# Kernel optimization log

Hardware: AMD Instinct MI355X
Metric: run time of the kernel (lower is better)

Reference implementation:

```python
import jax, jax.numpy as jnp
import numpy as np

DIM = 512
NUM_HEADS = 8
WINDOW = 8
HEAD_DIM = DIM // NUM_HEADS
SCALE = HEAD_DIM ** -0.5


def setup_inputs() -> dict:
    key = jax.random.key(0)
    ks = jax.random.split(key, 6)
    B, S, C = 16, 4096, DIM
    hidden_states = jax.random.normal(ks[0], (B, S, C), dtype=jnp.float32)
    attn_output = jnp.zeros((1,), dtype=jnp.float32)  # unused positional arg in original __call__
    # nn.Linear params stored as (in, out) for y = x @ W + b
    qkv_w = jax.random.normal(ks[1], (C, 3 * C), dtype=jnp.float32) * (C ** -0.5)
    qkv_b = jnp.zeros((3 * C,), dtype=jnp.float32)
    proj_w = jax.random.normal(ks[2], (C, C), dtype=jnp.float32) * (C ** -0.5)
    proj_b = jnp.zeros((C,), dtype=jnp.float32)
    return {
        "attn_output": attn_output,
        "hidden_states": hidden_states,
        "qkv_w": qkv_w,
        "qkv_b": qkv_b,
        "proj_w": proj_w,
        "proj_b": proj_b,
    }


def reference(attn_output, hidden_states, qkv_w, qkv_b, proj_w, proj_b):
    B, S, C = hidden_states.shape
    h = w = int(np.sqrt(S))
    ws = WINDOW
    nh, hd = NUM_HEADS, HEAD_DIM
    # [B, S, C] -> [B, h, w, C]; h, w divisible by ws so no padding needed.
    x = hidden_states.reshape(B, h, w, C)
    # window partition -> [B, Nwin, T, C], T = ws*ws
    x = x.reshape(B, h // ws, ws, w // ws, ws, C)
    x = x.transpose(0, 1, 3, 2, 4, 5).reshape(B, (h // ws) * (w // ws), ws * ws, C)
    Nwin, T = x.shape[1], x.shape[2]
    # QKV projection
    qkv = x @ qkv_w + qkv_b                      # [B, Nwin, T, 3C]
    qkv = qkv.reshape(B, Nwin, T, 3, nh, hd)
    q, k, v = qkv[..., 0, :, :], qkv[..., 1, :, :], qkv[..., 2, :, :]  # [B, Nwin, T, nh, hd]
    # attention within each window
    attn = jnp.einsum('bwthd,bwshd->bwhts', q, k) * SCALE
    attn = jax.nn.softmax(attn, axis=-1)
    out = jnp.einsum('bwhts,bwshd->bwthd', attn, v).reshape(B, Nwin, T, C)
    out = out @ proj_w + proj_b
    # window reassembly -> [B, h, w, C]
    out = out.reshape(B, h // ws, w // ws, ws, ws, C)
    out = out.transpose(0, 1, 3, 2, 4, 5).reshape(B, h, w, C)
    return out.reshape(B, S, C)
```

## Files before the change

### kernel.cpp

```cpp
#include <hip/hip_runtime.h>
#include <stdint.h>

typedef __attribute__((ext_vector_type(8))) __bf16 v8bf;
typedef __attribute__((ext_vector_type(4))) __bf16 v4bf;
typedef __attribute__((ext_vector_type(4))) float  v4f;

#define SCALE 0.125f

__device__ __forceinline__ unsigned short f2bf(float f) {
  unsigned u = __float_as_uint(f);
  u += 0x7fffu + ((u >> 16) & 1u);
  return (unsigned short)(u >> 16);
}

__global__ void __launch_bounds__(256) k_transpose_cast(
    const float* __restrict__ in, unsigned short* __restrict__ out, int K, int N) {
  __shared__ float tile[64][65];
  const int t  = threadIdx.x;
  const int kt = blockIdx.x * 64;
  const int nt = blockIdx.y * 64;
  {
    int kl = t >> 2;
    int c0 = (t & 3) * 16;
    const float* src = in + (size_t)(kt + kl) * N + nt + c0;
#pragma unroll
    for (int i = 0; i < 16; i += 4) {
      float4 v = *(const float4*)(src + i);
      tile[kl][c0 + i + 0] = v.x; tile[kl][c0 + i + 1] = v.y;
      tile[kl][c0 + i + 2] = v.z; tile[kl][c0 + i + 3] = v.w;
    }
  }
  __syncthreads();
  {
    int nl = t >> 2;
    int k0 = (t & 3) * 16;
    unsigned short* dst = out + (size_t)(nt + nl) * K + kt + k0;
#pragma unroll
    for (int i = 0; i < 16; ++i) dst[i] = f2bf(tile[k0 + i][nl]);
  }
}

__global__ void __launch_bounds__(256) k_gather_cast(
    const float* __restrict__ x, unsigned short* __restrict__ xg) {
  const int t  = threadIdx.x;
  const int m  = blockIdx.x * 4 + (t >> 6);
  const int i0 = (t & 63) * 8;
  const int b = m >> 12, r = m & 4095, win = r >> 6, tt = r & 63;
  const int y  = ((win >> 3) << 3) + (tt >> 3);
  const int xx = ((win & 7) << 3) + (tt & 7);
  const size_t s = ((size_t)b << 12) + (size_t)y * 64 + xx;
  const float4* src = (const float4*)(x + s * 512 + i0);
  float4 a = src[0], c = src[1];
  unsigned u0 = (unsigned)f2bf(a.x) | ((unsigned)f2bf(a.y) << 16);
  unsigned u1 = (unsigned)f2bf(a.z) | ((unsigned)f2bf(a.w) << 16);
  unsigned u2 = (unsigned)f2bf(c.x) | ((unsigned)f2bf(c.y) << 16);
  unsigned u3 = (unsigned)f2bf(c.z) | ((unsigned)f2bf(c.w) << 16);
  *(int4*)(xg + (size_t)m * 512 + i0) = make_int4((int)u0, (int)u1, (int)u2, (int)u3);
}

__device__ __forceinline__ void stage_tile(const unsigned short* g, int row0, int k0,
                                           unsigned short* s, int tid) {
#pragma unroll
  for (int p = 0; p < 2; ++p) {
    int o = p * 4096 + tid * 16;
    const char* src = (const char*)g + (((size_t)(row0 + (o >> 6))) << 10) + (k0 << 1) + (o & 63);
    char* dst = (char*)s + p * 4096 + (tid & ~63) * 16;
    __builtin_amdgcn_global_load_lds((const __attribute__((address_space(1))) void*)src,
                                     (__attribute__((address_space(3))) void*)dst, 16, 0, 0);
  }
}

__device__ __forceinline__ void gemm_core(const unsigned short* A, const unsigned short* Bt,
                                          int rowBase, int colBase,
                                          unsigned short* sA, unsigned short* sB,
                                          v4f acc[4][4]) {
  const int tid = threadIdx.x;
  const int lane = tid & 63, wid = tid >> 6;
  const int wr = wid >> 1, wc = wid & 1;
  const int la = lane & 15, lb = lane >> 4;
#pragma unroll 1
  for (int kt = 0; kt < 16; ++kt) {
    const int k0 = kt * 32;
    stage_tile(A,  rowBase, k0, sA, tid);
    stage_tile(Bt, colBase, k0, sB, tid);
    asm volatile("s_waitcnt vmcnt(0)" ::: "memory");
    __syncthreads();
    v8bf af[4], bf_[4];
#pragma unroll
    for (int m = 0; m < 4; ++m)
      af[m] = *(const v8bf*)&sA[(wr * 64 + m * 16 + la) * 32 + lb * 8];
#pragma unroll
    for (int n = 0; n < 4; ++n)
      bf_[n] = *(const v8bf*)&sB[(wc * 64 + n * 16 + la) * 32 + lb * 8];
#pragma unroll
    for (int m = 0; m < 4; ++m)
#pragma unroll
      for (int n = 0; n < 4; ++n)
        acc[m][n] = __builtin_amdgcn_mfma_f32_16x16x32_bf16(af[m], bf_[n], acc[m][n], 0, 0, 0);
    __syncthreads();
  }
}

__global__ void __launch_bounds__(256) k_gemm_qkv(
    const unsigned short* __restrict__ A, const unsigned short* __restrict__ Bt,
    const float* __restrict__ bias, unsigned short* __restrict__ C) {
  __shared__ unsigned short sA[128 * 32];
  __shared__ unsigned short sB[128 * 32];
  const int bid = blockIdx.x;
  const int b2 = (bid & 7) * 768 + (bid >> 3);
  const int tm = b2 / 12, tn = b2 % 12;
  const int rowBase = tm * 128, colBase = tn * 128;
  v4f acc[4][4] = {};
  gemm_core(A, Bt, rowBase, colBase, sA, sB, acc);
  const int tid = threadIdx.x, lane = tid & 63, wid = tid >> 6;
  const int wr = wid >> 1, wc = wid & 1, la = lane & 15, lb = lane >> 4;
#pragma unroll
  for (int n = 0; n < 4; ++n) {
    const int col = colBase + wc * 64 + n * 16 + la;
    const float bv = bias[col];
#pragma unroll
    for (int m = 0; m < 4; ++m)
#pragma unroll
      for (int j = 0; j < 4; ++j) {
        const size_t row = (size_t)rowBase + wr * 64 + m * 16 + lb * 4 + j;
        C[row * 1536 + col] = f2bf(acc[m][n][j] + bv);
      }
  }
}

__global__ void __launch_bounds__(256) k_gemm_proj(
    const unsigned short* __restrict__ A, const unsigned short* __restrict__ Bt,
    const float* __restrict__ bias, float* __restrict__ out) {
  __shared__ unsigned short sA[128 * 32];
  __shared__ unsigned short sB[128 * 32];
  const int bid = blockIdx.x;
  const int b2 = (bid & 7) * 256 + (bid >> 3);
  const int tm = b2 >> 2, tn = b2 & 3;
  const int rowBase = tm * 128, colBase = tn * 128;
  v4f acc[4][4] = {};
  gemm_core(A, Bt, rowBase, colBase, sA, sB, acc);
  const int tid = threadIdx.x, lane = tid & 63, wid = tid >> 6;
  const int wr = wid >> 1, wc = wid & 1, la = lane & 15, lb = lane >> 4;
#pragma unroll
  for (int m = 0; m < 4; ++m) {
#pragma unroll
    for (int j = 0; j < 4; ++j) {
      const int row = rowBase + wr * 64 + m * 16 + lb * 4 + j;
      const int b = row >> 12, r = row & 4095, win = r >> 6, tt = r & 63;
      const int y  = ((win >> 3) << 3) + (tt >> 3);
      const int xx = ((win & 7) << 3) + (tt & 7);
      const size_t srow = ((size_t)b << 12) + (size_t)y * 64 + xx;
      float* orow = out + srow * 512;
#pragma unroll
      for (int n = 0; n < 4; ++n) {
        const int col = colBase + wc * 64 + n * 16 + la;
        orow[col] = acc[m][n][j] + bias[col];
      }
    }
  }
}

__global__ void __launch_bounds__(256) k_attn(
    const unsigned short* __restrict__ QKV, unsigned short* __restrict__ O) {
  __shared__ unsigned short sQ[64 * 72];
  __shared__ unsigned short sK[64 * 72];
  __shared__ unsigned short sP[64 * 72];
  __shared__ unsigned short sVt[64 * 68];
  const int bid = blockIdx.x;
  const int b = bid >> 9, win = (bid >> 3) & 63, head = bid & 7;
  const size_t m0 = ((size_t)b << 12) + (size_t)win * 64;
  const int tid = threadIdx.x, lane = tid & 63, w = tid >> 6;
  const int la = lane & 15, lb = lane >> 4;

  {
    const int rowl = tid >> 2;
    const unsigned short* qrow = QKV + (m0 + rowl) * 1536;
#pragma unroll
    for (int p = 0; p < 2; ++p) {
      const int seg = (tid & 3) + p * 4;
      int4 vq = *(const int4*)(qrow + head * 64 + seg * 8);
      *(int4*)&sQ[rowl * 72 + seg * 8] = vq;
      int4 vk = *(const int4*)(qrow + 512 + head * 64 + seg * 8);
      *(int4*)&sK[rowl * 72 + seg * 8] = vk;
      int4 vv = *(const int4*)(qrow + 1024 + head * 64 + seg * 8);
      const unsigned short* pv = (const unsigned short*)&vv;
#pragma unroll
      for (int i = 0; i < 8; ++i)
        sVt[(seg * 8 + i) * 68 + rowl] = pv[i];
    }
  }
  __syncthreads();

  v4f sc[4] = {};
#pragma unroll
  for (int kk = 0; kk < 2; ++kk) {
    v8bf aq = *(const v8bf*)&sQ[(w * 16 + la) * 72 + kk * 32 + lb * 8];
#pragma unroll
    for (int n = 0; n < 4; ++n) {
      v8bf bk = *(const v8bf*)&sK[(n * 16 + la) * 72 + kk * 32 + lb * 8];
      sc[n] = __builtin_amdgcn_mfma_f32_16x16x32_bf16(aq, bk, sc[n], 0, 0, 0);
    }
  }
#pragma unroll
  for (int n = 0; n < 4; ++n) sc[n] *= SCALE;

  float mj[4], sj[4], pv_[4][4];
#pragma unroll
  for (int j = 0; j < 4; ++j) {
    float mx = fmaxf(fmaxf(sc[0][j], sc[1][j]), fmaxf(sc[2][j], sc[3][j]));
    mx = fmaxf(mx, __shfl_xor(mx, 1));
    mx = fmaxf(mx, __shfl_xor(mx, 2));
    mx = fmaxf(mx, __shfl_xor(mx, 4));
    mx = fmaxf(mx, __shfl_xor(mx, 8));
    mj[j] = mx;
  }
#pragma unroll
  for (int j = 0; j < 4; ++j) {
    float sum = 0.f;
#pragma unroll
    for (int n = 0; n < 4; ++n) { pv_[n][j] = __expf(sc[n][j] - mj[j]); sum += pv_[n][j]; }
    sum += __shfl_xor(sum, 1);
    sum += __shfl_xor(sum, 2);
    sum += __shfl_xor(sum, 4);
    sum += __shfl_xor(sum, 8);
    sj[j] = sum;
  }
#pragma unroll
  for (int n = 0; n < 4; ++n)
#pragma unroll
    for (int j = 0; j < 4; ++j)
      sP[(w * 16 + lb * 4 + j) * 72 + n * 16 + la] = f2bf(pv_[n][j]);

  v4f oa[4] = {};
#pragma unroll
  for (int kk = 0; kk < 2; ++kk) {
    v8bf ap = *(const v8bf*)&sP[(w * 16 + la) * 72 + kk * 32 + lb * 8];
#pragma unroll
    for (int n = 0; n < 4; ++n) {
      const int vidx = (n * 16 + la) * 68 + kk * 32 + lb * 8;
      v4bf lo = *(const v4bf*)&sVt[vidx];
      v4bf hi = *(const v4bf*)&sVt[vidx + 4];
      v8bf bv;
#pragma unroll
      for (int i = 0; i < 4; ++i) { bv[i] = lo[i]; bv[i + 4] = hi[i]; }
      oa[n] = __builtin_amdgcn_mfma_f32_16x16x32_bf16(ap, bv, oa[n], 0, 0, 0);
    }
  }
#pragma unroll
  for (int j = 0; j < 4; ++j) {
    const float inv = 1.0f / sj[j];
#pragma unroll
    for (int n = 0; n < 4; ++n)
      O[(m0 + w * 16 + lb * 4 + j) * 512 + head * 64 + n * 16 + la] = f2bf(oa[n][j] * inv);
  }
}

extern "C" void kernel_launch(void* const* d_in, const int* in_sizes, int n_in,
                              void* d_out, int out_size, void* d_ws, size_t ws_size,
                              hipStream_t stream) {
  const float* hidden = (const float*)d_in[1];
  const float* qkv_w  = (const float*)d_in[2];
  const float* qkv_b  = (const float*)d_in[3];
  const float* proj_w = (const float*)d_in[4];
  const float* proj_b = (const float*)d_in[5];
  float* out = (float*)d_out;

  char* ws = (char*)d_ws;
  unsigned short* QKV = (unsigned short*)(ws);
  unsigned short* Xg  = (unsigned short*)(ws + 201326592);
  unsigned short* Wq  = (unsigned short*)(ws + 268435456);
  unsigned short* Wp  = (unsigned short*)(ws + 270008320);
  if (ws_size < 270532608) return;
  unsigned short* Obuf = Xg;

  k_transpose_cast<<<dim3(8, 24), 256, 0, stream>>>(qkv_w, Wq, 512, 1536);
  k_transpose_cast<<<dim3(8, 8),  256, 0, stream>>>(proj_w, Wp, 512, 512);
  k_gather_cast<<<16384, 256, 0, stream>>>(hidden, Xg);
  k_gemm_qkv<<<6144, 256, 0, stream>>>(Xg, Wq, qkv_b, QKV);
  k_attn<<<8192, 256, 0, stream>>>(QKV, Obuf);
  k_gemm_proj<<<2048, 256, 0, stream>>>(Obuf, Wp, proj_b, out);
}
```

Before: 496.1 us.

## Replace LDS-staged GEMM with direct-global MFMA loads and 256x128 tiles

Drops the shared-memory staging and both per-k barriers in the QKV and projection GEMMs. Each wave now loads its MFMA operand fragments straight from global memory and computes a 64x128 sub-tile, so a block covers 256x128 and the grid is halved. Occupancy is hinted at 2 blocks per CU through launch bounds. This removes LDS traffic and synchronisation, but fragments are no longer shared between waves, so global and L2 traffic rise and the 16-byte strided loads may coalesce poorly.

```diff
diff --git a/kernel.cpp b/kernel.cpp
--- a/kernel.cpp
+++ b/kernel.cpp
@@ -58,106 +58,86 @@
   *(int4*)(xg + (size_t)m * 512 + i0) = make_int4((int)u0, (int)u1, (int)u2, (int)u3);
 }
 
-__device__ __forceinline__ void stage_tile(const unsigned short* g, int row0, int k0,
-                                           unsigned short* s, int tid) {
-#pragma unroll
-  for (int p = 0; p < 2; ++p) {
-    int o = p * 4096 + tid * 16;
-    const char* src = (const char*)g + (((size_t)(row0 + (o >> 6))) << 10) + (k0 << 1) + (o & 63);
-    char* dst = (char*)s + p * 4096 + (tid & ~63) * 16;
-    __builtin_amdgcn_global_load_lds((const __attribute__((address_space(1))) void*)src,
-                                     (__attribute__((address_space(3))) void*)dst, 16, 0, 0);
-  }
-}
-
-__device__ __forceinline__ void gemm_core(const unsigned short* A, const unsigned short* Bt,
-                                          int rowBase, int colBase,
-                                          unsigned short* sA, unsigned short* sB,
-                                          v4f acc[4][4]) {
-  const int tid = threadIdx.x;
-  const int lane = tid & 63, wid = tid >> 6;
-  const int wr = wid >> 1, wc = wid & 1;
+__device__ __forceinline__ void gemm_core(const unsigned short* __restrict__ A,
+                                          const unsigned short* __restrict__ Bt,
+                                          int wRow, int colBase, v4f (&acc)[4][8]) {
+  const int lane = threadIdx.x & 63;
   const int la = lane & 15, lb = lane >> 4;
-#pragma unroll 1
-  for (int kt = 0; kt < 16; ++kt) {
-    const int k0 = kt * 32;
-    stage_tile(A,  rowBase, k0, sA, tid);
-    stage_tile(Bt, colBase, k0, sB, tid);
-    asm volatile("s_waitcnt vmcnt(0)" ::: "memory");
-    __syncthreads();
-    v8bf af[4], bf_[4];
+  const unsigned short* ap = A  + (size_t)(wRow    + la) * 512 + lb * 8;
+  const unsigned short* bp = Bt + (size_t)(colBase + la) * 512 + lb * 8;
+#pragma unroll 2
+  for (int kk = 0; kk < 16; ++kk) {
+    v8bf a[4], b[8];
 #pragma unroll
     for (int m = 0; m < 4; ++m)
-      af[m] = *(const v8bf*)&sA[(wr * 64 + m * 16 + la) * 32 + lb * 8];
-#pragma unroll
-    for (int n = 0; n < 4; ++n)
-      bf_[n] = *(const v8bf*)&sB[(wc * 64 + n * 16 + la) * 32 + lb * 8];
+      a[m] = *(const v8bf*)(ap + kk * 32 + (size_t)m * 16 * 512);
+#pragma unroll
+    for (int n = 0; n < 8; ++n)
+      b[n] = *(const v8bf*)(bp + kk * 32 + (size_t)n * 16 * 512);
 #pragma unroll
     for (int m = 0; m < 4; ++m)
 #pragma unroll
-      for (int n = 0; n < 4; ++n)
-        acc[m][n] = __builtin_amdgcn_mfma_f32_16x16x32_bf16(af[m], bf_[n], acc[m][n], 0, 0, 0);
-    __syncthreads();
-  }
-}
-
-__global__ void __launch_bounds__(256) k_gemm_qkv(
+      for (int n = 0; n < 8; ++n)
+        acc[m][n] = __builtin_amdgcn_mfma_f32_16x16x32_bf16(a[m], b[n], acc[m][n], 0, 0, 0);
+  }
+}
+
+__global__ void __launch_bounds__(256, 2) k_gemm_qkv(
     const unsigned short* __restrict__ A, const unsigned short* __restrict__ Bt,
     const float* __restrict__ bias, unsigned short* __restrict__ C) {
-  __shared__ unsigned short sA[128 * 32];
-  __shared__ unsigned short sB[128 * 32];
   const int bid = blockIdx.x;
-  const int b2 = (bid & 7) * 768 + (bid >> 3);
-  const int tm = b2 / 12, tn = b2 % 12;
-  const int rowBase = tm * 128, colBase = tn * 128;
-  v4f acc[4][4] = {};
-  gemm_core(A, Bt, rowBase, colBase, sA, sB, acc);
-  const int tid = threadIdx.x, lane = tid & 63, wid = tid >> 6;
-  const int wr = wid >> 1, wc = wid & 1, la = lane & 15, lb = lane >> 4;
-#pragma unroll
-  for (int n = 0; n < 4; ++n) {
-    const int col = colBase + wc * 64 + n * 16 + la;
-    const float bv = bias[col];
-#pragma unroll
-    for (int m = 0; m < 4; ++m)
-#pragma unroll
-      for (int j = 0; j < 4; ++j) {
-        const size_t row = (size_t)rowBase + wr * 64 + m * 16 + lb * 4 + j;
-        C[row * 1536 + col] = f2bf(acc[m][n][j] + bv);
-      }
-  }
-}
-
-__global__ void __launch_bounds__(256) k_gemm_proj(
+  const int x = bid & 7, j = bid >> 3;
+  const int tm = x * 32 + j / 12, tn = j % 12;
+  const int wid = threadIdx.x >> 6;
+  const int wRow = tm * 256 + wid * 64;
+  const int colBase = tn * 128;
+  v4f acc[4][8] = {};
+  gemm_core(A, Bt, wRow, colBase, acc);
+  const int lane = threadIdx.x & 63, la = lane & 15, lb = lane >> 4;
+  float bv[8];
+#pragma unroll
+  for (int n = 0; n < 8; ++n) bv[n] = bias[colBase + n * 16 + la];
+#pragma unroll
+  for (int m = 0; m < 4; ++m)
+#pragma unroll
+    for (int jj = 0; jj < 4; ++jj) {
+      const size_t row = (size_t)wRow + m * 16 + lb * 4 + jj;
+      unsigned short* crow = C + row * 1536 + colBase + la;
+#pragma unroll
+      for (int n = 0; n < 8; ++n)
+        crow[n * 16] = f2bf(acc[m][n][jj] + bv[n]);
+    }
+}
+
+__global__ void __launch_bounds__(256, 2) k_gemm_proj(
     const unsigned short* __restrict__ A, const unsigned short* __restrict__ Bt,
     const float* __restrict__ bias, float* __restrict__ out) {
-  __shared__ unsigned short sA[128 * 32];
-  __shared__ unsigned short sB[128 * 32];
   const int bid = blockIdx.x;
-  const int b2 = (bid & 7) * 256 + (bid >> 3);
-  const int tm = b2 >> 2, tn = b2 & 3;
-  const int rowBase = tm * 128, colBase = tn * 128;
-  v4f acc[4][4] = {};
-  gemm_core(A, Bt, rowBase, colBase, sA, sB, acc);
-  const int tid = threadIdx.x, lane = tid & 63, wid = tid >> 6;
-  const int wr = wid >> 1, wc = wid & 1, la = lane & 15, lb = lane >> 4;
-#pragma unroll
-  for (int m = 0; m < 4; ++m) {
-#pragma unroll
-    for (int j = 0; j < 4; ++j) {
-      const int row = rowBase + wr * 64 + m * 16 + lb * 4 + j;
+  const int x = bid & 7, j = bid >> 3;
+  const int tm = x * 32 + j / 4, tn = j & 3;
+  const int wid = threadIdx.x >> 6;
+  const int wRow = tm * 256 + wid * 64;
+  const int colBase = tn * 128;
+  v4f acc[4][8] = {};
+  gemm_core(A, Bt, wRow, colBase, acc);
+  const int lane = threadIdx.x & 63, la = lane & 15, lb = lane >> 4;
+  float bv[8];
+#pragma unroll
+  for (int n = 0; n < 8; ++n) bv[n] = bias[colBase + n * 16 + la];
+#pragma unroll
+  for (int m = 0; m < 4; ++m)
+#pragma unroll
+    for (int jj = 0; jj < 4; ++jj) {
+      const int row = wRow + m * 16 + lb * 4 + jj;
       const int b = row >> 12, r = row & 4095, win = r >> 6, tt = r & 63;
       const int y  = ((win >> 3) << 3) + (tt >> 3);
       const int xx = ((win & 7) << 3) + (tt & 7);
       const size_t srow = ((size_t)b << 12) + (size_t)y * 64 + xx;
-      float* orow = out + srow * 512;
-#pragma unroll
-      for (int n = 0; n < 4; ++n) {
-        const int col = colBase + wc * 64 + n * 16 + la;
-        orow[col] = acc[m][n][j] + bias[col];
-      }
-    }
-  }
+      float* orow = out + srow * 512 + colBase + la;
+#pragma unroll
+      for (int n = 0; n < 8; ++n)
+        orow[n * 16] = acc[m][n][jj] + bv[n];
+    }
 }
 
 __global__ void __launch_bounds__(256) k_attn(
@@ -276,7 +256,7 @@
   k_transpose_cast<<<dim3(8, 24), 256, 0, stream>>>(qkv_w, Wq, 512, 1536);
   k_transpose_cast<<<dim3(8, 8),  256, 0, stream>>>(proj_w, Wp, 512, 512);
   k_gather_cast<<<16384, 256, 0, stream>>>(hidden, Xg);
-  k_gemm_qkv<<<6144, 256, 0, stream>>>(Xg, Wq, qkv_b, QKV);
+  k_gemm_qkv<<<3072, 256, 0, stream>>>(Xg, Wq, qkv_b, QKV);
   k_attn<<<8192, 256, 0, stream>>>(QKV, Obuf);
-  k_gemm_proj<<<2048, 256, 0, stream>>>(Obuf, Wp, proj_b, out);
-}
+  k_gemm_proj<<<1024, 256, 0, stream>>>(Obuf, Wp, proj_b, out);
+}
```

After: 672.1 us. +35.5%, slower.

## Double-buffer GEMM LDS tiles and alias attention P buffer onto Q

Applied to the files above, without the earlier changes.

The shared GEMM mainloop now uses two LDS buffers per operand. It issues the global-to-LDS loads for the next K tile before running the MFMAs on the current one, and drops the per-iteration explicit vmcnt wait, so memory latency can overlap compute. This doubles GEMM LDS use per block, and correctness now relies on the barrier to order the async LDS writes. The attention kernel also reuses the Q buffer for the softmax probabilities instead of a separate array, cutting LDS footprint. That is only safe if Q is no longer read when P is written.

```diff
diff --git a/kernel.cpp b/kernel.cpp
--- a/kernel.cpp
+++ b/kernel.cpp
@@ -72,40 +72,48 @@
 
 __device__ __forceinline__ void gemm_core(const unsigned short* A, const unsigned short* Bt,
                                           int rowBase, int colBase,
-                                          unsigned short* sA, unsigned short* sB,
-                                          v4f acc[4][4]) {
+                                          unsigned short (&sA)[2][4096],
+                                          unsigned short (&sB)[2][4096],
+                                          v4f (&acc)[4][4]) {
   const int tid = threadIdx.x;
   const int lane = tid & 63, wid = tid >> 6;
   const int wr = wid >> 1, wc = wid & 1;
   const int la = lane & 15, lb = lane >> 4;
+
+  stage_tile(A,  rowBase, 0, sA[0], tid);
+  stage_tile(Bt, colBase, 0, sB[0], tid);
+  __syncthreads();
+
+  int cur = 0;
 #pragma unroll 1
   for (int kt = 0; kt < 16; ++kt) {
-    const int k0 = kt * 32;
-    stage_tile(A,  rowBase, k0, sA, tid);
-    stage_tile(Bt, colBase, k0, sB, tid);
-    asm volatile("s_waitcnt vmcnt(0)" ::: "memory");
-    __syncthreads();
+    if (kt < 15) {
+      const int k1 = (kt + 1) * 32;
+      stage_tile(A,  rowBase, k1, sA[cur ^ 1], tid);
+      stage_tile(Bt, colBase, k1, sB[cur ^ 1], tid);
+    }
     v8bf af[4], bf_[4];
 #pragma unroll
     for (int m = 0; m < 4; ++m)
-      af[m] = *(const v8bf*)&sA[(wr * 64 + m * 16 + la) * 32 + lb * 8];
+      af[m] = *(const v8bf*)&sA[cur][(wr * 64 + m * 16 + la) * 32 + lb * 8];
 #pragma unroll
     for (int n = 0; n < 4; ++n)
-      bf_[n] = *(const v8bf*)&sB[(wc * 64 + n * 16 + la) * 32 + lb * 8];
+      bf_[n] = *(const v8bf*)&sB[cur][(wc * 64 + n * 16 + la) * 32 + lb * 8];
 #pragma unroll
     for (int m = 0; m < 4; ++m)
 #pragma unroll
       for (int n = 0; n < 4; ++n)
         acc[m][n] = __builtin_amdgcn_mfma_f32_16x16x32_bf16(af[m], bf_[n], acc[m][n], 0, 0, 0);
     __syncthreads();
+    cur ^= 1;
   }
 }
 
 __global__ void __launch_bounds__(256) k_gemm_qkv(
     const unsigned short* __restrict__ A, const unsigned short* __restrict__ Bt,
     const float* __restrict__ bias, unsigned short* __restrict__ C) {
-  __shared__ unsigned short sA[128 * 32];
-  __shared__ unsigned short sB[128 * 32];
+  __shared__ unsigned short sA[2][4096];
+  __shared__ unsigned short sB[2][4096];
   const int bid = blockIdx.x;
   const int b2 = (bid & 7) * 768 + (bid >> 3);
   const int tm = b2 / 12, tn = b2 % 12;
@@ -131,8 +139,8 @@
 __global__ void __launch_bounds__(256) k_gemm_proj(
     const unsigned short* __restrict__ A, const unsigned short* __restrict__ Bt,
     const float* __restrict__ bias, float* __restrict__ out) {
-  __shared__ unsigned short sA[128 * 32];
-  __shared__ unsigned short sB[128 * 32];
+  __shared__ unsigned short sA[2][4096];
+  __shared__ unsigned short sB[2][4096];
   const int bid = blockIdx.x;
   const int b2 = (bid & 7) * 256 + (bid >> 3);
   const int tm = b2 >> 2, tn = b2 & 3;
@@ -164,8 +172,8 @@
     const unsigned short* __restrict__ QKV, unsigned short* __restrict__ O) {
   __shared__ unsigned short sQ[64 * 72];
   __shared__ unsigned short sK[64 * 72];
-  __shared__ unsigned short sP[64 * 72];
   __shared__ unsigned short sVt[64 * 68];
+  unsigned short* sP = sQ;
   const int bid = blockIdx.x;
   const int b = bid >> 9, win = (bid >> 3) & 63, head = bid & 7;
   const size_t m0 = ((size_t)b << 12) + (size_t)win * 64;
```

Measured after the change: 489.0 us. About the same (-1.4%).
